# Kernel optimization log

Hardware: AMD Instinct MI355X
Metric: run time of the kernel (lower is better)

## Reference

```python
import jax, jax.numpy as jnp
import numpy as np

B, S, D, H, HD, F = 2, 2048, 1024, 16, 64, 4096
EPS = 1e-5


def layer_norm(x, g, b):
    m = jnp.mean(x, axis=-1, keepdims=True)
    v = jnp.var(x, axis=-1, keepdims=True)
    return (x - m) * jax.lax.rsqrt(v + EPS) * g + b


def setup_inputs() -> dict:
    key = jax.random.key(0)
    ks = jax.random.split(key, 8)
    hidden_states = jax.random.normal(ks[0], (B, S, D), dtype=jnp.float32)
    # additive causal mask: 0 where allowed, -1e9 where masked
    causal = jnp.tril(jnp.ones((S, S), dtype=bool))
    attention_mask = jnp.where(causal, 0.0, -1e9).astype(jnp.float32)[None, None]
    sd = 1.0 / np.sqrt(D)
    Wq = jax.random.normal(ks[1], (D, D), jnp.float32) * sd
    Wk = jax.random.normal(ks[2], (D, D), jnp.float32) * sd
    Wv = jax.random.normal(ks[3], (D, D), jnp.float32) * sd
    Wo = jax.random.normal(ks[4], (D, D), jnp.float32) * sd
    W1 = jax.random.normal(ks[5], (D, F), jnp.float32) * sd
    W2 = jax.random.normal(ks[6], (F, D), jnp.float32) * (1.0 / np.sqrt(F))
    ln1_g = jnp.ones((D,), jnp.float32)
    ln1_b = jnp.zeros((D,), jnp.float32)
    ln2_g = jnp.ones((D,), jnp.float32)
    ln2_b = jnp.zeros((D,), jnp.float32)
    return dict(hidden_states=hidden_states, attention_mask=attention_mask,
                ln1_g=ln1_g, ln1_b=ln1_b, Wq=Wq, Wk=Wk, Wv=Wv, Wo=Wo,
                ln2_g=ln2_g, ln2_b=ln2_b, W1=W1, W2=W2)


def reference(hidden_states, attention_mask, ln1_g, ln1_b, Wq, Wk, Wv, Wo,
              ln2_g, ln2_b, W1, W2):
    x = hidden_states
    # --- attention sublayer (pre-LN) ---
    h = layer_norm(x, ln1_g, ln1_b)
    q = (h @ Wq).reshape(B, S, H, HD).transpose(0, 2, 1, 3)  # b h s d
    k = (h @ Wk).reshape(B, S, H, HD).transpose(0, 2, 1, 3)
    v = (h @ Wv).reshape(B, S, H, HD).transpose(0, 2, 1, 3)
    scores = jnp.einsum('bhqd,bhkd->bhqk', q, k) / np.sqrt(HD)
    scores = scores + attention_mask
    attn = jax.nn.softmax(scores, axis=-1)
    ctx = jnp.einsum('bhqk,bhkd->bhqd', attn, v)
    ctx = ctx.transpose(0, 2, 1, 3).reshape(B, S, D)
    x = x + ctx @ Wo
    # --- FFN sublayer (pre-LN) ---
    h = layer_norm(x, ln2_g, ln2_b)
    h = jax.nn.gelu(h @ W1, approximate=False) @ W2
    out = x + h
    return out, k, v
```

## Files before the change

### kernel.cpp

```cpp
#include <hip/hip_runtime.h>
#include <hip/hip_bf16.h>
#include <cstdint>
#include <cstddef>

#define BB 2
#define SS 2048
#define DD 1024
#define HH 16
#define HDIM 64
#define FF 4096
#define RR (BB*SS)

typedef __attribute__((ext_vector_type(8))) short short8;
typedef __attribute__((ext_vector_type(4))) float floatx4;

__device__ __forceinline__ unsigned short f2bf(float f){
    __hip_bfloat16 h = __float2bfloat16(f);
    return *reinterpret_cast<unsigned short*>(&h);
}

__device__ __forceinline__ void load_lds16(const void* g, void* l){
    __builtin_amdgcn_global_load_lds((__attribute__((address_space(1))) void*)g,
                                     (__attribute__((address_space(3))) void*)l, 16, 0, 0);
}


template<int BN, int EPI>
__global__ __launch_bounds__(256) void gemm_bt(const unsigned short* __restrict__ A,
                                               const unsigned short* __restrict__ B,
                                               int M, int N, int K,
                                               float* __restrict__ cf,
                                               const float* __restrict__ resid,
                                               unsigned short* __restrict__ cbf,
                                               unsigned short* __restrict__ qb,
                                               float* __restrict__ kout,
                                               unsigned short* __restrict__ kbf,
                                               float* __restrict__ vout)
{
    constexpr int MI_M = (BN==128) ? 4 : 2;
    __shared__ unsigned short As[128*64];
    __shared__ unsigned short Bs[BN*64];
    const int tid  = threadIdx.x;
    const int lane = tid & 63;
    const int wave = tid >> 6;
    const int quad = lane >> 4, l15 = lane & 15;
    const int wrow = (BN==128) ? (wave>>1)*64 : wave*32;
    const int wcol = (BN==128) ? (wave&1)*64 : 0;
    const int gm0 = blockIdx.y * 128, gn0 = blockIdx.x * BN;

    floatx4 acc[MI_M][4];
#pragma unroll
    for (int i=0;i<MI_M;i++)
#pragma unroll
        for (int j=0;j<4;j++) acc[i][j] = (floatx4){0.f,0.f,0.f,0.f};

    const int rsub = lane >> 3;
    const int d8   = (lane & 7) * 8;
    const int ksub = ((lane & 7) ^ rsub) * 8;
    constexpr int nchw = (128 + BN) / 32;

    for (int kt = 0; kt < K; kt += 64) {
#pragma unroll
        for (int i=0;i<nchw;i++){
            int c = wave*nchw + i;
            if (c < 16)
                load_lds16(A + (size_t)(gm0 + c*8 + rsub)*K + kt + ksub,
                           As + c*512 + rsub*64 + d8);
            else
                load_lds16(B + (size_t)(gn0 + (c-16)*8 + rsub)*K + kt + ksub,
                           Bs + (c-16)*512 + rsub*64 + d8);
        }
        __syncthreads();
#pragma unroll
        for (int kk=0; kk<64; kk+=32){
            const int cb4 = kk >> 3;
            short8 af[MI_M], bfr[4];
#pragma unroll
            for (int mi=0;mi<MI_M;mi++){
                int row = wrow + mi*16 + l15;
                af[mi] = *(const short8*)&As[row*64 + (((cb4+quad) ^ (row&7)))*8];
            }
#pragma unroll
            for (int ni=0;ni<4;ni++){
                int row = wcol + ni*16 + l15;
                bfr[ni] = *(const short8*)&Bs[row*64 + (((cb4+quad) ^ (row&7)))*8];
            }
#pragma unroll
            for (int mi=0;mi<MI_M;mi++)
#pragma unroll
                for (int ni=0;ni<4;ni++)
                    acc[mi][ni] = __builtin_amdgcn_mfma_f32_16x16x32_bf16(af[mi], bfr[ni], acc[mi][ni], 0, 0, 0);
        }
        __syncthreads();
    }

#pragma unroll
    for (int mi=0;mi<MI_M;mi++)
#pragma unroll
        for (int ni=0;ni<4;ni++)
#pragma unroll
            for (int r=0;r<4;r++){
                int row = gm0 + wrow + mi*16 + quad*4 + r;
                int col = gn0 + wcol + ni*16 + l15;
                float v = acc[mi][ni][r];
                if constexpr (EPI == 1){
                    int region = gn0 >> 10;
                    if (region == 0){
                        qb[(size_t)row*1024 + col] = f2bf(v);
                    } else {
                        int c1 = col & 1023;
                        int h = c1 >> 6, d = c1 & 63;
                        int b = row >> 11, s = row & (SS-1);
                        size_t o = ((size_t)((b*HH + h)*SS + s))*HDIM + d;
                        if (region == 1){ kout[o] = v; kbf[o] = f2bf(v); }
                        else            { vout[o] = v; }
                    }
                } else if constexpr (EPI == 2){
                    size_t o = (size_t)row*N + col;
                    cf[o] = v + resid[o];
                } else {
                    float g = 0.5f*v*(1.f + erff(v*0.70710678118f));
                    cbf[(size_t)row*N + col] = f2bf(g);
                }
            }
}

__global__ __launch_bounds__(256) void attn_kernel(const unsigned short* __restrict__ qbf,
                                                   const unsigned short* __restrict__ kbf,
                                                   const unsigned short* __restrict__ vtbf,
                                                   unsigned short* __restrict__ ctx)
{
    __shared__ unsigned short Ks[2][64*64];
    __shared__ unsigned short Vs[2][64*64];
    __shared__ unsigned short Ps[4][16*64];
    const int tid  = threadIdx.x;
    const int lane = tid & 63;
    const int wave = tid >> 6;
    const int quad = lane >> 4, l15 = lane & 15;
    const int aqt = blockIdx.x;
    const int bqt = 31 - aqt;
    const int bh = blockIdx.y;
    const int b = bh >> 4, h = bh & 15;
    const int q0a = aqt * 64, q0b = bqt * 64;

    const unsigned short* kb  = kbf  + (size_t)bh * SS * HDIM;
    const unsigned short* vtb = vtbf + (size_t)bh * HDIM * SS;

    const unsigned short* qra = qbf + (size_t)(b*SS + q0a + wave*16 + l15)*DD + h*HDIM + quad*8;
    const unsigned short* qrb = qbf + (size_t)(b*SS + q0b + wave*16 + l15)*DD + h*HDIM + quad*8;
    short8 qa0 = *(const short8*)qra;
    short8 qa1 = *(const short8*)(qra + 32);
    short8 qb0 = *(const short8*)qrb;
    short8 qb1 = *(const short8*)(qrb + 32);

    float lpA[4] = {0.f,0.f,0.f,0.f}, lpB[4] = {0.f,0.f,0.f,0.f};
    floatx4 accA[4], accB[4];
#pragma unroll
    for (int n=0;n<4;n++){ accA[n] = (floatx4){0.f,0.f,0.f,0.f}; accB[n] = (floatx4){0.f,0.f,0.f,0.f}; }

    const int r8 = lane >> 3;
    const int c8 = ((lane & 7) ^ r8) * 8;
    const int d8 = (lane & 7) * 8;
    const int nkt = bqt + 1;
    const float SC = 0.125f * 1.44269504f;

#pragma unroll
    for (int p=0;p<2;p++){
        int row = p*32 + wave*8 + r8;
        load_lds16(kb  + (size_t)row*HDIM + c8,  &Ks[0][row*64 + d8]);
        load_lds16(vtb + (size_t)row*SS   + c8,  &Vs[0][row*64 + d8]);
    }

    unsigned short* pl = Ps[wave];
    int cur = 0;
    for (int kt=0; kt<nkt; kt++){
        __syncthreads();
        if (kt+1 < nkt){
            int nb = cur ^ 1;
#pragma unroll
            for (int p=0;p<2;p++){
                int row = p*32 + wave*8 + r8;
                load_lds16(kb  + (size_t)((kt+1)*64 + row)*HDIM + c8, &Ks[nb][row*64 + d8]);
                load_lds16(vtb + (size_t)row*SS + (size_t)(kt+1)*64 + c8, &Vs[nb][row*64 + d8]);
            }
        }
        const unsigned short* ks = Ks[cur];
        const unsigned short* vs = Vs[cur];

        short8 kf0[4], kf1[4];
#pragma unroll
        for (int j=0;j<4;j++){
            int row = j*16 + l15;
            kf0[j] = *(const short8*)&ks[row*64 + ((quad     ^ (row&7)))*8];
            kf1[j] = *(const short8*)&ks[row*64 + (((quad+4) ^ (row&7)))*8];
        }
        short8 vf0[4], vf1[4];
#pragma unroll
        for (int n=0;n<4;n++){
            int row = n*16 + l15;
            vf0[n] = *(const short8*)&vs[row*64 + ((quad     ^ (row&7)))*8];
            vf1[n] = *(const short8*)&vs[row*64 + (((quad+4) ^ (row&7)))*8];
        }

        {
            floatx4 s[4];
#pragma unroll
            for (int j=0;j<4;j++){
                floatx4 z = (floatx4){0.f,0.f,0.f,0.f};
                z = __builtin_amdgcn_mfma_f32_16x16x32_bf16(qb0, kf0[j], z, 0, 0, 0);
                z = __builtin_amdgcn_mfma_f32_16x16x32_bf16(qb1, kf1[j], z, 0, 0, 0);
                s[j] = z;
            }
#pragma unroll
            for (int j=0;j<4;j++)
#pragma unroll
                for (int r=0;r<4;r++){
                    int prow = quad*4 + r;
                    float p = exp2f(s[j][r]*SC);
                    if (kt == bqt){
                        int row = q0b + wave*16 + prow;
                        int col = kt*64 + j*16 + l15;
                        if (col > row) p = 0.f;
                    }
                    lpB[r] += p;
                    int ch = (2*j + (l15>>3)) ^ (prow&7);
                    pl[prow*64 + ch*8 + (l15&7)] = f2bf(p);
                }
            short8 pf0 = *(const short8*)&pl[l15*64 + ((quad     ^ (l15&7)))*8];
            short8 pf1 = *(const short8*)&pl[l15*64 + (((quad+4) ^ (l15&7)))*8];
#pragma unroll
            for (int n=0;n<4;n++){
                accB[n] = __builtin_amdgcn_mfma_f32_16x16x32_bf16(pf0, vf0[n], accB[n], 0, 0, 0);
                accB[n] = __builtin_amdgcn_mfma_f32_16x16x32_bf16(pf1, vf1[n], accB[n], 0, 0, 0);
            }
        }

        if (kt <= aqt){
            floatx4 s[4];
#pragma unroll
            for (int j=0;j<4;j++){
                floatx4 z = (floatx4){0.f,0.f,0.f,0.f};
                z = __builtin_amdgcn_mfma_f32_16x16x32_bf16(qa0, kf0[j], z, 0, 0, 0);
                z = __builtin_amdgcn_mfma_f32_16x16x32_bf16(qa1, kf1[j], z, 0, 0, 0);
                s[j] = z;
            }
#pragma unroll
            for (int j=0;j<4;j++)
#pragma unroll
                for (int r=0;r<4;r++){
                    int prow = quad*4 + r;
                    float p = exp2f(s[j][r]*SC);
                    if (kt == aqt){
                        int row = q0a + wave*16 + prow;
                        int col = kt*64 + j*16 + l15;
                        if (col > row) p = 0.f;
                    }
                    lpA[r] += p;
                    int ch = (2*j + (l15>>3)) ^ (prow&7);
                    pl[prow*64 + ch*8 + (l15&7)] = f2bf(p);
                }
            short8 pf0 = *(const short8*)&pl[l15*64 + ((quad     ^ (l15&7)))*8];
            short8 pf1 = *(const short8*)&pl[l15*64 + (((quad+4) ^ (l15&7)))*8];
#pragma unroll
            for (int n=0;n<4;n++){
                accA[n] = __builtin_amdgcn_mfma_f32_16x16x32_bf16(pf0, vf0[n], accA[n], 0, 0, 0);
                accA[n] = __builtin_amdgcn_mfma_f32_16x16x32_bf16(pf1, vf1[n], accA[n], 0, 0, 0);
            }
        }
        cur ^= 1;
    }

#pragma unroll
    for (int r=0;r<4;r++){
        float va = lpA[r], vb = lpB[r];
        va += __shfl_xor(va, 1); vb += __shfl_xor(vb, 1);
        va += __shfl_xor(va, 2); vb += __shfl_xor(vb, 2);
        va += __shfl_xor(va, 4); vb += __shfl_xor(vb, 4);
        va += __shfl_xor(va, 8); vb += __shfl_xor(vb, 8);
        lpA[r] = va; lpB[r] = vb;
    }
#pragma unroll
    for (int n=0;n<4;n++)
#pragma unroll
        for (int r=0;r<4;r++){
            float oa = accA[n][r] / lpA[r];
            float ob = accB[n][r] / lpB[r];
            ctx[(size_t)(b*SS + q0a + wave*16 + quad*4 + r)*DD + h*HDIM + n*16 + l15] = f2bf(oa);
            ctx[(size_t)(b*SS + q0b + wave*16 + quad*4 + r)*DD + h*HDIM + n*16 + l15] = f2bf(ob);
        }
}

__global__ __launch_bounds__(256) void ln_kernel(const float* __restrict__ x,
                                                 const float* __restrict__ g,
                                                 const float* __restrict__ bparm,
                                                 unsigned short* __restrict__ out)
{
    __shared__ float red[8];
    const int row = blockIdx.x;
    const int tid = threadIdx.x;
    const float* xr = x + (size_t)row*DD;
    float4 v = *(const float4*)(xr + tid*4);
    float s  = v.x+v.y+v.z+v.w;
    float sq = v.x*v.x + v.y*v.y + v.z*v.z + v.w*v.w;
#pragma unroll
    for (int off=1; off<64; off<<=1){ s += __shfl_xor(s, off); sq += __shfl_xor(sq, off); }
    if ((tid & 63) == 0){ red[tid>>6] = s; red[4 + (tid>>6)] = sq; }
    __syncthreads();
    float ts = red[0]+red[1]+red[2]+red[3];
    float tq = red[4]+red[5]+red[6]+red[7];
    float mean = ts * (1.f/DD);
    float var  = tq * (1.f/DD) - mean*mean;
    float inv  = rsqrtf(var + 1e-5f);
    float4 gv = *(const float4*)(g + tid*4);
    float4 bv = *(const float4*)(bparm + tid*4);
    ushort4 o;
    o.x = f2bf((v.x-mean)*inv*gv.x + bv.x);
    o.y = f2bf((v.y-mean)*inv*gv.y + bv.y);
    o.z = f2bf((v.z-mean)*inv*gv.z + bv.z);
    o.w = f2bf((v.w-mean)*inv*gv.w + bv.w);
    *(ushort4*)(out + (size_t)row*DD + tid*4) = o;
}

__global__ __launch_bounds__(256) void castT_kernel(const float* __restrict__ in,
                                                    unsigned short* __restrict__ out,
                                                    int R, int C)
{
    __shared__ float t[32][33];
    const size_t zoff = (size_t)blockIdx.z * R * C;
    in  += zoff; out += zoff;
    const int tr = blockIdx.y*32, tc = blockIdx.x*32;
    const int lr = threadIdx.x >> 5, lc = threadIdx.x & 31;
#pragma unroll
    for (int i=0;i<4;i++)
        t[lr + i*8][lc] = in[(size_t)(tr + lr + i*8)*C + tc + lc];
    __syncthreads();
#pragma unroll
    for (int i=0;i<4;i++)
        out[(size_t)(tc + lr + i*8)*R + tr + lc] = f2bf(t[lc][lr + i*8]);
}

extern "C" void kernel_launch(void* const* d_in, const int* in_sizes, int n_in,
                              void* d_out, int out_size, void* d_ws, size_t ws_size,
                              hipStream_t stream)
{
    const float* x     = (const float*)d_in[0];
    const float* ln1_g = (const float*)d_in[2];
    const float* ln1_b = (const float*)d_in[3];
    const float* Wq    = (const float*)d_in[4];
    const float* Wk    = (const float*)d_in[5];
    const float* Wv    = (const float*)d_in[6];
    const float* Wo    = (const float*)d_in[7];
    const float* ln2_g = (const float*)d_in[8];
    const float* ln2_b = (const float*)d_in[9];
    const float* W1    = (const float*)d_in[10];
    const float* W2    = (const float*)d_in[11];

    float* out  = (float*)d_out;
    float* kout = out  + (size_t)RR*DD;
    float* vout = kout + (size_t)BB*HH*SS*HDIM;

    char* w = (char*)d_ws;
    auto alloc = [&](size_t bytes) -> char* {
        char* p = w; w += (bytes + 255) & ~(size_t)255; return p;
    };
    unsigned short* qkvT  = (unsigned short*)alloc((size_t)3072*1024*2);
    unsigned short* WoT   = (unsigned short*)alloc((size_t)1024*1024*2);
    unsigned short* W1T   = (unsigned short*)alloc((size_t)4096*1024*2);
    unsigned short* W2T   = (unsigned short*)alloc((size_t)1024*4096*2);
    unsigned short* h_bf  = (unsigned short*)alloc((size_t)RR*DD*2);
    unsigned short* q_bf  = (unsigned short*)alloc((size_t)RR*DD*2);
    unsigned short* k_bf  = (unsigned short*)alloc((size_t)RR*DD*2);
    unsigned short* vt_bf = (unsigned short*)alloc((size_t)RR*DD*2);
    unsigned short* ctx_bf= (unsigned short*)alloc((size_t)RR*DD*2);
    unsigned short* act_bf= (unsigned short*)alloc((size_t)RR*FF*2);
    float* x1     = (float*)alloc((size_t)RR*DD*4);

    castT_kernel<<<dim3(32,32,1),  256, 0, stream>>>(Wq, qkvT,               1024, 1024);
    castT_kernel<<<dim3(32,32,1),  256, 0, stream>>>(Wk, qkvT + 1024*1024,   1024, 1024);
    castT_kernel<<<dim3(32,32,1),  256, 0, stream>>>(Wv, qkvT + 2*1024*1024, 1024, 1024);
    castT_kernel<<<dim3(32,32,1),  256, 0, stream>>>(Wo, WoT,                1024, 1024);
    castT_kernel<<<dim3(128,32,1), 256, 0, stream>>>(W1, W1T,                1024, 4096);
    castT_kernel<<<dim3(32,128,1), 256, 0, stream>>>(W2, W2T,                4096, 1024);

    ln_kernel<<<RR, 256, 0, stream>>>(x, ln1_g, ln1_b, h_bf);
    gemm_bt<128,1><<<dim3(3072/128, RR/128), 256, 0, stream>>>(
        h_bf, qkvT, RR, 3072, 1024, nullptr, nullptr, nullptr, q_bf, kout, k_bf, vout);
    castT_kernel<<<dim3(2, 64, BB*HH), 256, 0, stream>>>(vout, vt_bf, SS, HDIM);
    attn_kernel<<<dim3(16, BB*HH), 256, 0, stream>>>(q_bf, k_bf, vt_bf, ctx_bf);
    gemm_bt<64,2><<<dim3(1024/64, RR/128), 256, 0, stream>>>(
        ctx_bf, WoT, RR, 1024, 1024, x1, x, nullptr, nullptr, nullptr, nullptr, nullptr);

    ln_kernel<<<RR, 256, 0, stream>>>(x1, ln2_g, ln2_b, h_bf);
    gemm_bt<128,3><<<dim3(4096/128, RR/128), 256, 0, stream>>>(
        h_bf, W1T, RR, 4096, 1024, nullptr, nullptr, act_bf, nullptr, nullptr, nullptr, nullptr);
    gemm_bt<64,2><<<dim3(1024/64, RR/128), 256, 0, stream>>>(
        act_bf, W2T, RR, 1024, 4096, out, x1, nullptr, nullptr, nullptr, nullptr, nullptr);
}
```

Baseline: 388.9 us.

## Split-K the W2 FFN GEMM with 128-wide tiles and merge weight-cast launches

The final FFN down-projection (K=4096) now uses 128x128 tiles with a two-way split over K. Each split writes fp32 partials, and a separate combine kernel adds both partials plus the residual. The grid size stays the same while each tile gets more reuse. The four 1024x1024 weight transpose-casts are merged into one launch. The cost is an extra 2x16MB partial write/read pass and one more kernel launch.

```diff
diff --git a/kernel.cpp b/kernel.cpp
--- a/kernel.cpp
+++ b/kernel.cpp
@@ -28,7 +28,7 @@
 template<int BN, int EPI>
 __global__ __launch_bounds__(256) void gemm_bt(const unsigned short* __restrict__ A,
                                                const unsigned short* __restrict__ B,
-                                               int M, int N, int K,
+                                               int M, int N, int K, int KS,
                                                float* __restrict__ cf,
                                                const float* __restrict__ resid,
                                                unsigned short* __restrict__ cbf,
@@ -47,6 +47,7 @@
     const int wrow = (BN==128) ? (wave>>1)*64 : wave*32;
     const int wcol = (BN==128) ? (wave&1)*64 : 0;
     const int gm0 = blockIdx.y * 128, gn0 = blockIdx.x * BN;
+    const int k0 = blockIdx.z * KS, k1 = k0 + KS;
 
     floatx4 acc[MI_M][4];
 #pragma unroll
@@ -59,7 +60,7 @@
     const int ksub = ((lane & 7) ^ rsub) * 8;
     constexpr int nchw = (128 + BN) / 32;
 
-    for (int kt = 0; kt < K; kt += 64) {
+    for (int kt = k0; kt < k1; kt += 64) {
 #pragma unroll
         for (int i=0;i<nchw;i++){
             int c = wave*nchw + i;
@@ -118,11 +119,26 @@
                 } else if constexpr (EPI == 2){
                     size_t o = (size_t)row*N + col;
                     cf[o] = v + resid[o];
-                } else {
+                } else if constexpr (EPI == 3){
                     float g = 0.5f*v*(1.f + erff(v*0.70710678118f));
                     cbf[(size_t)row*N + col] = f2bf(g);
+                } else {
+                    cf[(size_t)blockIdx.z*M*N + (size_t)row*N + col] = v;
                 }
             }
+}
+
+__global__ __launch_bounds__(256) void combine2_kernel(const float* __restrict__ p0,
+                                                       const float* __restrict__ p1,
+                                                       const float* __restrict__ resid,
+                                                       float* __restrict__ out, int n4)
+{
+    const int i = blockIdx.x*256 + threadIdx.x;
+    if (i >= n4) return;
+    float4 a = ((const float4*)p0)[i];
+    float4 b = ((const float4*)p1)[i];
+    float4 c = ((const float4*)resid)[i];
+    ((float4*)out)[i] = make_float4(a.x+b.x+c.x, a.y+b.y+c.y, a.z+b.z+c.z, a.w+b.w+c.w);
 }
 
 __global__ __launch_bounds__(256) void attn_kernel(const unsigned short* __restrict__ qbf,
@@ -339,6 +355,30 @@
         out[(size_t)(tc + lr + i*8)*R + tr + lc] = f2bf(t[lc][lr + i*8]);
 }
 
+__global__ __launch_bounds__(256) void castT4_kernel(const float* __restrict__ i0,
+                                                     const float* __restrict__ i1,
+                                                     const float* __restrict__ i2,
+                                                     const float* __restrict__ i3,
+                                                     unsigned short* __restrict__ o0,
+                                                     unsigned short* __restrict__ o1,
+                                                     unsigned short* __restrict__ o2,
+                                                     unsigned short* __restrict__ o3)
+{
+    __shared__ float t[32][33];
+    const int z = blockIdx.z;
+    const float* in = (z==0) ? i0 : (z==1) ? i1 : (z==2) ? i2 : i3;
+    unsigned short* out = (z==0) ? o0 : (z==1) ? o1 : (z==2) ? o2 : o3;
+    const int tr = blockIdx.y*32, tc = blockIdx.x*32;
+    const int lr = threadIdx.x >> 5, lc = threadIdx.x & 31;
+#pragma unroll
+    for (int i=0;i<4;i++)
+        t[lr + i*8][lc] = in[(size_t)(tr + lr + i*8)*1024 + tc + lc];
+    __syncthreads();
+#pragma unroll
+    for (int i=0;i<4;i++)
+        out[(size_t)(tc + lr + i*8)*1024 + tr + lc] = f2bf(t[lc][lr + i*8]);
+}
+
 extern "C" void kernel_launch(void* const* d_in, const int* in_sizes, int n_in,
                               void* d_out, int out_size, void* d_ws, size_t ws_size,
                               hipStream_t stream)
@@ -374,25 +414,26 @@
     unsigned short* ctx_bf= (unsigned short*)alloc((size_t)RR*DD*2);
     unsigned short* act_bf= (unsigned short*)alloc((size_t)RR*FF*2);
     float* x1     = (float*)alloc((size_t)RR*DD*4);
-
-    castT_kernel<<<dim3(32,32,1),  256, 0, stream>>>(Wq, qkvT,               1024, 1024);
-    castT_kernel<<<dim3(32,32,1),  256, 0, stream>>>(Wk, qkvT + 1024*1024,   1024, 1024);
-    castT_kernel<<<dim3(32,32,1),  256, 0, stream>>>(Wv, qkvT + 2*1024*1024, 1024, 1024);
-    castT_kernel<<<dim3(32,32,1),  256, 0, stream>>>(Wo, WoT,                1024, 1024);
-    castT_kernel<<<dim3(128,32,1), 256, 0, stream>>>(W1, W1T,                1024, 4096);
-    castT_kernel<<<dim3(32,128,1), 256, 0, stream>>>(W2, W2T,                4096, 1024);
+    float* fpart  = (float*)alloc((size_t)2*RR*DD*4);
+
+    castT4_kernel<<<dim3(32,32,4), 256, 0, stream>>>(
+        Wq, Wk, Wv, Wo, qkvT, qkvT + 1024*1024, qkvT + 2*1024*1024, WoT);
+    castT_kernel<<<dim3(128,32,1), 256, 0, stream>>>(W1, W1T, 1024, 4096);
+    castT_kernel<<<dim3(32,128,1), 256, 0, stream>>>(W2, W2T, 4096, 1024);
 
     ln_kernel<<<RR, 256, 0, stream>>>(x, ln1_g, ln1_b, h_bf);
     gemm_bt<128,1><<<dim3(3072/128, RR/128), 256, 0, stream>>>(
-        h_bf, qkvT, RR, 3072, 1024, nullptr, nullptr, nullptr, q_bf, kout, k_bf, vout);
+        h_bf, qkvT, RR, 3072, 1024, 1024, nullptr, nullptr, nullptr, q_bf, kout, k_bf, vout);
     castT_kernel<<<dim3(2, 64, BB*HH), 256, 0, stream>>>(vout, vt_bf, SS, HDIM);
     attn_kernel<<<dim3(16, BB*HH), 256, 0, stream>>>(q_bf, k_bf, vt_bf, ctx_bf);
     gemm_bt<64,2><<<dim3(1024/64, RR/128), 256, 0, stream>>>(
-        ctx_bf, WoT, RR, 1024, 1024, x1, x, nullptr, nullptr, nullptr, nullptr, nullptr);
+        ctx_bf, WoT, RR, 1024, 1024, 1024, x1, x, nullptr, nullptr, nullptr, nullptr, nullptr);
 
     ln_kernel<<<RR, 256, 0, stream>>>(x1, ln2_g, ln2_b, h_bf);
     gemm_bt<128,3><<<dim3(4096/128, RR/128), 256, 0, stream>>>(
-        h_bf, W1T, RR, 4096, 1024, nullptr, nullptr, act_bf, nullptr, nullptr, nullptr, nullptr);
-    gemm_bt<64,2><<<dim3(1024/64, RR/128), 256, 0, stream>>>(
-        act_bf, W2T, RR, 1024, 4096, out, x1, nullptr, nullptr, nullptr, nullptr, nullptr);
-}
+        h_bf, W1T, RR, 4096, 1024, 1024, nullptr, nullptr, act_bf, nullptr, nullptr, nullptr, nullptr);
+    gemm_bt<128,4><<<dim3(1024/128, RR/128, 2), 256, 0, stream>>>(
+        act_bf, W2T, RR, 1024, 4096, 2048, fpart, nullptr, nullptr, nullptr, nullptr, nullptr, nullptr);
+    combine2_kernel<<<(RR*DD/4 + 255)/256, 256, 0, stream>>>(
+        fpart, fpart + (size_t)RR*DD, x1, out, RR*DD/4);
+}
```

New measurement: 380.1 us. -2.3%, faster.
